# Kernel optimization log

Measured on AMD Instinct MI355X. Metric: run time of the kernel, lower is better.

The kernel has to match this reference:

```python
import jax, jax.numpy as jnp
import numpy as np

N_NODES = 1024; DEG = 24; K_NN = 12
C_S = 384; C_Z = 128; C_G = 16; N_RBF = 64
N_EDGES = N_NODES * DEG          # 24576
N_EE = N_EDGES * K_NN            # 294912 edge-edge pairs
LN_EPS = 1e-5
RBF_MIN, RBF_MAX = 0.0, 20.0


def _layernorm(x, w, b):
    m = x.mean(-1, keepdims=True)
    v = ((x - m) ** 2).mean(-1, keepdims=True)
    return (x - m) * jax.lax.rsqrt(v + LN_EPS) * w + b


def setup_inputs() -> dict:
    key = jax.random.key(0)
    ks = iter(jax.random.split(key, 40))

    def lin(i, o):
        w = jax.random.normal(next(ks), (i, o), jnp.float32) / np.sqrt(i)
        b = jax.random.normal(next(ks), (o,), jnp.float32) * 0.01
        return w, b

    node_features = jax.random.normal(next(ks), (N_NODES, C_S), jnp.float32)
    node_trans = jax.random.normal(next(ks), (N_NODES, 3), jnp.float32) * 10.0
    edge_features = jax.random.normal(next(ks), (N_EDGES, C_Z), jnp.float32)

    # edge_index sorted by destination (column 1), fixed in-degree DEG per node
    rng = np.random.default_rng(0)
    dst = np.repeat(np.arange(N_NODES), DEG)
    src = rng.integers(0, N_NODES, size=N_EDGES)
    edge_index = jnp.asarray(np.stack([src, dst]), jnp.int32)

    # edge-edge kNN graph: each edge paired with K_NN other edges sharing the
    # same destination node (mirrors knn_graph(..., batch=sorted_edge_index[1]))
    t = np.arange(N_EDGES)
    base = (t // DEG) * DEG
    off = t % DEG
    nbr = base[:, None] + (off[:, None] + 1 + np.arange(K_NN)[None, :]) % DEG  # [E,K]
    edge_edge_index = jnp.asarray(
        np.stack([nbr.reshape(-1), np.repeat(t, K_NN)]), jnp.int32)  # [2, N_EE]

    ln_w = jnp.ones((C_Z,), jnp.float32); ln_b = jnp.zeros((C_Z,), jnp.float32)
    wl_w, wl_b = lin(C_S, C_G)
    wr_w, wr_b = lin(C_S, C_G)
    ep_w, ep_b = lin(C_Z, C_Z)
    eg_w, eg_b = lin(C_Z, C_Z)
    dg_w, dg_b = lin(C_G * C_G, C_Z)
    dp_w, dp_b = lin(N_RBF, C_Z)
    lno_w = jnp.ones((C_Z,), jnp.float32); lno_b = jnp.zeros((C_Z,), jnp.float32)
    lo_w, lo_b = lin(C_Z, C_Z)
    og_w, og_b = lin(C_Z, C_Z)

    return dict(node_features=node_features, node_trans=node_trans,
                edge_features=edge_features,
                ln_w=ln_w, ln_b=ln_b, wl_w=wl_w, wl_b=wl_b, wr_w=wr_w, wr_b=wr_b,
                ep_w=ep_w, ep_b=ep_b, eg_w=eg_w, eg_b=eg_b,
                dg_w=dg_w, dg_b=dg_b, dp_w=dp_w, dp_b=dp_b,
                lno_w=lno_w, lno_b=lno_b, lo_w=lo_w, lo_b=lo_b,
                og_w=og_w, og_b=og_b,
                edge_index=edge_index, edge_edge_index=edge_edge_index)


def reference(node_features, node_trans, edge_features,
              ln_w, ln_b, wl_w, wl_b, wr_w, wr_b,
              ep_w, ep_b, eg_w, eg_b, dg_w, dg_b, dp_w, dp_b,
              lno_w, lno_b, lo_w, lo_b, og_w, og_b,
              edge_index, edge_edge_index):
    eps = 1e-8
    src = edge_index[0]
    eei0, eei1 = edge_edge_index[0], edge_edge_index[1]
    n1 = src[eei1]  # source node of target edge of each pair
    n2 = src[eei0]  # source node of source edge of each pair

    ef = _layernorm(edge_features, ln_w, ln_b)            # [E, c_z]
    nl = node_features @ wl_w + wl_b                      # [N, c_g]
    nr = node_features @ wr_w + wr_b                      # [N, c_g]

    # per-pair outer product, flattened: [N_EE, c_g*c_g]
    e3 = (nl[n1][:, :, None] * nr[n2][:, None, :]).reshape(-1, C_G * C_G)
    gate3 = e3 @ dg_w + dg_b                              # [N_EE, c_z]

    d = jnp.linalg.norm(node_trans[n1] - node_trans[n2] + eps, axis=-1)
    mu = jnp.linspace(RBF_MIN, RBF_MAX, N_RBF)
    sigma = (RBF_MAX - RBF_MIN) / N_RBF
    rbf = jnp.exp(-(((d[:, None] - mu) / sigma) ** 2))    # [N_EE, num_rbf]
    e3f = jax.nn.sigmoid(gate3) * (rbf @ dp_w + dp_b)

    e2 = jax.nn.sigmoid(ef @ eg_w + eg_b) * (ef @ ep_w + ep_b)  # [E, c_z]
    upd = e2[eei0] * e3f                                  # [N_EE, c_z]
    upd = jax.ops.segment_sum(upd, eei0, num_segments=N_EDGES)  # [E, c_z]

    upd = _layernorm(upd, lno_w, lno_b) @ lo_w + lo_b
    upd = upd * jax.nn.sigmoid(ef @ og_w + og_b)
    return upd
```

## Files before the change

kernel.cpp:

```cpp
#include <hip/hip_runtime.h>
#include <math.h>

#define N_NODES 1024
#define DEG     24
#define K_NN    12
#define C_S     384
#define C_Z     128
#define C_G     16
#define N_RBF   64
#define N_EDGES (N_NODES*DEG)

typedef short short8 __attribute__((ext_vector_type(8)));
typedef float f32x4  __attribute__((ext_vector_type(4)));

__device__ __forceinline__ float sigf(float x) {
  return __builtin_amdgcn_rcpf(1.f + __expf(-x));
}

__device__ __forceinline__ short f2b(float x) {
  union { float f; unsigned u; } v; v.f = x;
  unsigned r = v.u + 0x7FFFu + ((v.u >> 16) & 1u);
  return (short)(r >> 16);
}
__device__ __forceinline__ float b2f(short s) {
  union { unsigned u; float f; } v; v.u = ((unsigned)(unsigned short)s) << 16;
  return v.f;
}

__global__ __launch_bounds__(256) void k_prep(
    const float* __restrict__ nf, const float* __restrict__ wl_w, const float* __restrict__ wl_b,
    const float* __restrict__ wr_w, const float* __restrict__ wr_b,
    const float* __restrict__ dg_w,
    float* __restrict__ nl, short* __restrict__ At)
{
  __shared__ float rows[4][C_S];
  __shared__ float nrv[4][C_G];
  int b = blockIdx.x, t = threadIdx.x;
  for (int v = t; v < 4*C_S; v += 256) rows[v/C_S][v%C_S] = nf[(size_t)b*4*C_S + v];
  __syncthreads();
  {
    int nd = t >> 6, lt = t & 63;
    int c = lt >> 1, jseg = lt & 1, cc = c & 15;
    const float* w = (c < 16) ? wl_w : wr_w;
    float acc = 0.f;
    #pragma unroll 8
    for (int j = jseg*192; j < jseg*192 + 192; ++j) acc += rows[nd][j] * w[j*C_G + cc];
    acc += __shfl_xor(acc, 1);
    if (jseg == 0) {
      float v = acc + ((c < 16) ? wl_b[cc] : wr_b[cc]);
      if (c < 16) nl[(b*4 + nd)*C_G + cc] = v;
      else nrv[nd][cc] = v;
    }
  }
  __syncthreads();
  {
    int c2 = t & 127, ih = t >> 7;
    float a4[4][8];
    #pragma unroll
    for (int nd = 0; nd < 4; ++nd)
      #pragma unroll
      for (int q = 0; q < 8; ++q) a4[nd][q] = 0.f;
    for (int j = 0; j < C_G; ++j) {
      float w8[8];
      #pragma unroll
      for (int q = 0; q < 8; ++q) w8[q] = dg_w[(size_t)((ih*8 + q)*C_G + j)*C_Z + c2];
      #pragma unroll
      for (int nd = 0; nd < 4; ++nd) {
        float nv = nrv[nd][j];
        #pragma unroll
        for (int q = 0; q < 8; ++q) a4[nd][q] += nv * w8[q];
      }
    }
    #pragma unroll
    for (int nd = 0; nd < 4; ++nd) {
      short8 o8;
      #pragma unroll
      for (int q = 0; q < 8; ++q) o8[q] = f2b(a4[nd][q]);
      *(short8*)&At[(size_t)(b*4 + nd)*2048 + c2*16 + ih*8] = o8;
    }
  }
}

__global__ __launch_bounds__(256) void k_wts(
    const float* __restrict__ eg, const float* __restrict__ ep,
    const float* __restrict__ og, const float* __restrict__ lo,
    const float* __restrict__ dp_w,
    short* __restrict__ wT, short* __restrict__ dpT)
{
  int b = blockIdx.x, t = threadIdx.x;
  if (b == 64) {
    int c2 = t & 127, rh = t >> 7;
    for (int r = rh*36; r < rh*36 + 36; ++r)
      dpT[c2*72 + r] = (r < 64) ? f2b(dp_w[r*128 + c2]) : (short)0;
    return;
  }
  __shared__ float tb[32][33];
  int w = b >> 4; int tile = b & 15;
  int bi = tile >> 2, bj = tile & 3;
  const float* src = (w == 0) ? eg : (w == 1) ? ep : (w == 2) ? og : lo;
  short* dst = wT + w * 16384;
  int c = t & 31, r0 = t >> 5;
  #pragma unroll
  for (int p = 0; p < 4; ++p) { int r = r0 + p*8; tb[r][c] = src[(bi*32 + r)*128 + bj*32 + c]; }
  __syncthreads();
  #pragma unroll
  for (int p = 0; p < 4; ++p) { int r = r0 + p*8; dst[(bj*32 + r)*128 + bi*32 + c] = f2b(tb[c][r]); }
}

__global__ __launch_bounds__(384) void k_gates(
    const float* __restrict__ efin, const float* __restrict__ ln_w, const float* __restrict__ ln_b,
    const short* __restrict__ wT,
    const float* __restrict__ eg_b, const float* __restrict__ ep_b, const float* __restrict__ og_b,
    float* __restrict__ e2, short* __restrict__ ogs)
{
  __shared__ short xn[6*16*136];
  int t = threadIdx.x;
  int wv = t >> 6, lane = t & 63;
  int col = lane & 15, grp = lane >> 4;
  int ebase = blockIdx.x * 96 + wv * 16;
  int row = col, c0 = grp * 32;
  float x[32];
  {
    size_t ein = (size_t)(ebase + row) * C_Z + c0;
    #pragma unroll
    for (int q = 0; q < 8; ++q) {
      float4 v = *(const float4*)(efin + ein + q*4);
      x[q*4+0]=v.x; x[q*4+1]=v.y; x[q*4+2]=v.z; x[q*4+3]=v.w;
    }
  }
  float s = 0.f;
  #pragma unroll
  for (int q = 0; q < 32; ++q) s += x[q];
  s += __shfl_xor(s, 16); s += __shfl_xor(s, 32);
  float mean = s * (1.f/128.f);
  float vs = 0.f;
  #pragma unroll
  for (int q = 0; q < 32; ++q) { float d = x[q]-mean; vs += d*d; }
  vs += __shfl_xor(vs, 16); vs += __shfl_xor(vs, 32);
  float rstd = rsqrtf(vs*(1.f/128.f) + 1e-5f);
  short* xw = &xn[wv*2176 + row*136 + c0];
  #pragma unroll
  for (int h = 0; h < 4; ++h) {
    short8 o;
    #pragma unroll
    for (int j = 0; j < 8; ++j) {
      int idx = h*8 + j;
      o[j] = f2b((x[idx]-mean)*rstd*ln_w[c0+idx] + ln_b[c0+idx]);
    }
    *(short8*)(xw + h*8) = o;
  }
  __syncthreads();
  short8 a[4];
  const short* xr = &xn[wv*2176 + col*136];
  #pragma unroll
  for (int ks = 0; ks < 4; ++ks) a[ks] = *(const short8*)(xr + ks*32 + grp*8);
  #pragma unroll
  for (int h = 0; h < 8; ++h) {
    int ch = col + 16*h;
    f32x4 acc = (f32x4){0.f,0.f,0.f,0.f}, acc2 = (f32x4){0.f,0.f,0.f,0.f};
    #pragma unroll
    for (int ks = 0; ks < 4; ++ks)
      acc = __builtin_amdgcn_mfma_f32_16x16x32_bf16(
          a[ks], *(const short8*)(wT + (size_t)ch*128 + ks*32 + grp*8), acc, 0, 0, 0);
    #pragma unroll
    for (int ks = 0; ks < 4; ++ks)
      acc2 = __builtin_amdgcn_mfma_f32_16x16x32_bf16(
          a[ks], *(const short8*)(wT + 16384 + (size_t)ch*128 + ks*32 + grp*8), acc2, 0, 0, 0);
    float egb = eg_b[ch], epb = ep_b[ch];
    #pragma unroll
    for (int r = 0; r < 4; ++r) {
      size_t e = (size_t)(ebase + grp*4 + r);
      e2[e*C_Z + ch] = sigf(acc[r] + egb) * (acc2[r] + epb);
    }
  }
  #pragma unroll
  for (int h = 0; h < 8; ++h) {
    int ch = col + 16*h;
    f32x4 acc = (f32x4){0.f,0.f,0.f,0.f};
    #pragma unroll
    for (int ks = 0; ks < 4; ++ks)
      acc = __builtin_amdgcn_mfma_f32_16x16x32_bf16(
          a[ks], *(const short8*)(wT + 32768 + (size_t)ch*128 + ks*32 + grp*8), acc, 0, 0, 0);
    float ogb = og_b[ch];
    #pragma unroll
    for (int r = 0; r < 4; ++r) {
      size_t e = (size_t)(ebase + grp*4 + r);
      ogs[e*C_Z + ch] = f2b(sigf(acc[r] + ogb));
    }
  }
}

__global__ __launch_bounds__(256) void k_pairs2(
    const int* __restrict__ eidx, const float* __restrict__ pos,
    const float* __restrict__ nl, const short* __restrict__ At, const short* __restrict__ dpTg,
    const float* __restrict__ dg_b, const float* __restrict__ dp_b,
    const float* __restrict__ e2, const float* __restrict__ lno_w, const float* __restrict__ lno_b,
    short* __restrict__ Un)
{
  __shared__ float p4[DEG][4];
  __shared__ int   s24[DEG];
  __shared__ short nlb[DEG*C_G];
  int t = threadIdx.x;
  int g = blockIdx.x / 6, sub = blockIdx.x - g*6;
  if (t < DEG) {
    int s = eidx[g*DEG + t];
    s24[t] = s;
    p4[t][0] = pos[s*3+0]; p4[t][1] = pos[s*3+1]; p4[t][2] = pos[s*3+2]; p4[t][3] = 0.f;
  }
  __syncthreads();
  for (int v = t; v < DEG*C_G; v += 256)
    nlb[v] = f2b(nl[s24[v>>4]*C_G + (v & 15)]);
  __syncthreads();

  int wv = t >> 6, lane = t & 63, col = lane & 15, grp = lane >> 4;
  int o = sub*4 + wv;

  float dgb[8], dpb[8];
  #pragma unroll
  for (int q = 0; q < 8; ++q) { int c = col+16*q; dgb[q] = dg_b[c]; dpb[q] = dp_b[c]; }
  const float RS = 3.2f, MUS = 20.f/63.f;

  int n2 = s24[o];
  int o2 = o - 1 - col; if (o2 < 0) o2 += DEG;
  bool vk = (col < K_NN);
  float d;
  {
    float dx = p4[o2][0]-p4[o][0]+1e-8f;
    float dy = p4[o2][1]-p4[o][1]+1e-8f;
    float dz = p4[o2][2]-p4[o][2]+1e-8f;
    d = vk ? sqrtf(dx*dx+dy*dy+dz*dz) : 1.0e6f;
  }
  short8 zz = {0,0,0,0,0,0,0,0};
  short8 a_nl = zz;
  if (vk && grp < 2) a_nl = *(const short8*)&nlb[o2*C_G + grp*8];
  short8 a_r0, a_r1;
  #pragma unroll
  for (int j = 0; j < 8; ++j) {
    float z0 = (d - (float)(grp*8 + j)*MUS)*RS;
    float z1 = (d - (float)(32 + grp*8 + j)*MUS)*RS;
    a_r0[j] = f2b(__expf(-z0*z0));
    a_r1[j] = f2b(__expf(-z1*z1));
  }
  const short8* Ab = (const short8*)(At + (size_t)n2*2048);
  float v1 = 0.f, v2 = 0.f;
  #pragma unroll
  for (int cb = 0; cb < 8; ++cb) {
    f32x4 accg = (f32x4){0.f,0.f,0.f,0.f};
    f32x4 accd = (f32x4){0.f,0.f,0.f,0.f};
    short8 b = (grp < 2) ? Ab[(col+16*cb)*2 + grp] : zz;
    accg = __builtin_amdgcn_mfma_f32_16x16x32_bf16(a_nl, b, accg, 0, 0, 0);
    const short* dbase = dpTg + (col+16*cb)*72 + grp*8;
    accd = __builtin_amdgcn_mfma_f32_16x16x32_bf16(a_r0, *(const short8*)dbase,      accd, 0, 0, 0);
    accd = __builtin_amdgcn_mfma_f32_16x16x32_bf16(a_r1, *(const short8*)(dbase+32), accd, 0, 0, 0);
    float sacc = 0.f;
    #pragma unroll
    for (int r = 0; r < 4; ++r)
      sacc += sigf(accg[r] + dgb[cb]) * (accd[r] + dpb[cb]);
    sacc = (grp == 3) ? 0.f : sacc;
    sacc += __shfl_xor(sacc, 16); sacc += __shfl_xor(sacc, 32);
    v1 = (cb == grp)     ? sacc : v1;
    v2 = (cb == grp + 4) ? sacc : v2;
  }
  size_t e = (size_t)(g*DEG + o);
  v1 *= e2[e*C_Z + lane];
  v2 *= e2[e*C_Z + 64 + lane];
  float s = v1 + v2;
  s += __shfl_xor(s,1); s += __shfl_xor(s,2); s += __shfl_xor(s,4);
  s += __shfl_xor(s,8); s += __shfl_xor(s,16); s += __shfl_xor(s,32);
  float mean = s * (1.f/128.f);
  float d1 = v1 - mean, d2 = v2 - mean;
  float vsum = d1*d1 + d2*d2;
  vsum += __shfl_xor(vsum,1); vsum += __shfl_xor(vsum,2); vsum += __shfl_xor(vsum,4);
  vsum += __shfl_xor(vsum,8); vsum += __shfl_xor(vsum,16); vsum += __shfl_xor(vsum,32);
  float rstd = rsqrtf(vsum*(1.f/128.f) + 1e-5f);
  Un[e*C_Z + lane]      = f2b(d1*rstd*lno_w[lane]      + lno_b[lane]);
  Un[e*C_Z + 64 + lane] = f2b(d2*rstd*lno_w[64 + lane] + lno_b[64 + lane]);
}

__global__ __launch_bounds__(256) void k_out2(
    const short* __restrict__ Un, const short* __restrict__ wTlo, const float* __restrict__ lo_b,
    const short* __restrict__ ogs, float* __restrict__ out)
{
  int t = threadIdx.x, wv = t >> 6, lane = t & 63, col = lane & 15, grp = lane >> 4;
  int ebase = blockIdx.x * 64 + wv * 16;
  short8 ua[4];
  #pragma unroll
  for (int ks = 0; ks < 4; ++ks)
    ua[ks] = *(const short8*)(Un + (size_t)(ebase + col)*C_Z + ks*32 + grp*8);
  #pragma unroll
  for (int h = 0; h < 8; ++h) {
    int ch = col + 16*h;
    f32x4 oacc = (f32x4){0.f,0.f,0.f,0.f};
    #pragma unroll
    for (int ks = 0; ks < 4; ++ks)
      oacc = __builtin_amdgcn_mfma_f32_16x16x32_bf16(
          ua[ks], *(const short8*)(wTlo + (size_t)ch*128 + ks*32 + grp*8), oacc, 0, 0, 0);
    float lob = lo_b[ch];
    #pragma unroll
    for (int r = 0; r < 4; ++r) {
      size_t e = (size_t)(ebase + grp*4 + r);
      out[e*C_Z + ch] = (oacc[r] + lob) * b2f(ogs[e*C_Z + ch]);
    }
  }
}

extern "C" void kernel_launch(void* const* d_in, const int* in_sizes, int n_in,
                              void* d_out, int out_size, void* d_ws, size_t ws_size,
                              hipStream_t stream)
{
  const float* nf    = (const float*)d_in[0];
  const float* pos   = (const float*)d_in[1];
  const float* efin  = (const float*)d_in[2];
  const float* ln_w  = (const float*)d_in[3];
  const float* ln_b  = (const float*)d_in[4];
  const float* wl_w  = (const float*)d_in[5];
  const float* wl_b  = (const float*)d_in[6];
  const float* wr_w  = (const float*)d_in[7];
  const float* wr_b  = (const float*)d_in[8];
  const float* ep_w  = (const float*)d_in[9];
  const float* ep_b  = (const float*)d_in[10];
  const float* eg_w  = (const float*)d_in[11];
  const float* eg_b  = (const float*)d_in[12];
  const float* dg_w  = (const float*)d_in[13];
  const float* dg_b  = (const float*)d_in[14];
  const float* dp_w  = (const float*)d_in[15];
  const float* dp_b  = (const float*)d_in[16];
  const float* lno_w = (const float*)d_in[17];
  const float* lno_b = (const float*)d_in[18];
  const float* lo_w  = (const float*)d_in[19];
  const float* lo_b  = (const float*)d_in[20];
  const float* og_w  = (const float*)d_in[21];
  const float* og_b  = (const float*)d_in[22];
  const int*   eidx  = (const int*)d_in[23];

  float* ws   = (float*)d_ws;
  float* nlw  = ws;
  short* Atw  = (short*)(ws + 32768);
  short* dpTw = (short*)(ws + 32768 + 1048576);
  short* wTw  = (short*)(ws + 32768 + 1048576 + 8192);
  float* e2w  = ws + 1122304;
  short* ogw  = (short*)(ws + 4268032);
  short* Unw  = (short*)(ws + 5840896);
  float* outp = (float*)d_out;

  k_prep  <<<256, 256, 0, stream>>>(nf, wl_w, wl_b, wr_w, wr_b, dg_w, nlw, Atw);
  k_wts   <<<65, 256, 0, stream>>>(eg_w, ep_w, og_w, lo_w, dp_w, wTw, dpTw);
  k_gates <<<256, 384, 0, stream>>>(efin, ln_w, ln_b, wTw, eg_b, ep_b, og_b, e2w, ogw);
  k_pairs2<<<6144, 256, 0, stream>>>(eidx, pos, nlw, Atw, dpTw, dg_b, dp_b,
                                     e2w, lno_w, lno_b, Unw);
  k_out2  <<<384, 256, 0, stream>>>(Unw, wTw + 49152, lo_b, ogw, outp);
}
```

Measured before the change: 113.5 us.

## Fuse edge gates, pair aggregation and output projection into one kernel

Merges the gating kernel, pair kernel and output kernel into a single per-edge kernel. Each block of 4 edges does its input layernorm, the eg/ep/og projections, the pair aggregation and the output projection, keeping intermediates in shared memory. This removes the global round trips for e2, og and Un plus two launches. The cost is that the MFMA tiles now use only 4 of 16 rows, wasting matrix throughput and reloading the weight matrices per block. The nl buffer is also stored as bf16.

```diff
diff --git a/kernel.cpp b/kernel.cpp
--- a/kernel.cpp
+++ b/kernel.cpp
@@ -31,7 +31,7 @@
     const float* __restrict__ nf, const float* __restrict__ wl_w, const float* __restrict__ wl_b,
     const float* __restrict__ wr_w, const float* __restrict__ wr_b,
     const float* __restrict__ dg_w,
-    float* __restrict__ nl, short* __restrict__ At)
+    short* __restrict__ nlB, short* __restrict__ At)
 {
   __shared__ float rows[4][C_S];
   __shared__ float nrv[4][C_G];
@@ -48,7 +48,7 @@
     acc += __shfl_xor(acc, 1);
     if (jseg == 0) {
       float v = acc + ((c < 16) ? wl_b[cc] : wr_b[cc]);
-      if (c < 16) nl[(b*4 + nd)*C_G + cc] = v;
+      if (c < 16) nlB[(b*4 + nd)*C_G + cc] = f2b(v);
       else nrv[nd][cc] = v;
     }
   }
@@ -107,101 +107,29 @@
   for (int p = 0; p < 4; ++p) { int r = r0 + p*8; dst[(bj*32 + r)*128 + bi*32 + c] = f2b(tb[c][r]); }
 }
 
-__global__ __launch_bounds__(384) void k_gates(
+__global__ __launch_bounds__(256) void k_mega(
     const float* __restrict__ efin, const float* __restrict__ ln_w, const float* __restrict__ ln_b,
     const short* __restrict__ wT,
     const float* __restrict__ eg_b, const float* __restrict__ ep_b, const float* __restrict__ og_b,
-    float* __restrict__ e2, short* __restrict__ ogs)
+    const int* __restrict__ eidx, const float* __restrict__ pos,
+    const short* __restrict__ nlB, const short* __restrict__ At, const short* __restrict__ dpTg,
+    const float* __restrict__ dg_b, const float* __restrict__ dp_b,
+    const float* __restrict__ lno_w, const float* __restrict__ lno_b, const float* __restrict__ lo_b,
+    float* __restrict__ out)
 {
-  __shared__ short xn[6*16*136];
-  int t = threadIdx.x;
-  int wv = t >> 6, lane = t & 63;
-  int col = lane & 15, grp = lane >> 4;
-  int ebase = blockIdx.x * 96 + wv * 16;
-  int row = col, c0 = grp * 32;
-  float x[32];
-  {
-    size_t ein = (size_t)(ebase + row) * C_Z + c0;
-    #pragma unroll
-    for (int q = 0; q < 8; ++q) {
-      float4 v = *(const float4*)(efin + ein + q*4);
-      x[q*4+0]=v.x; x[q*4+1]=v.y; x[q*4+2]=v.z; x[q*4+3]=v.w;
-    }
-  }
-  float s = 0.f;
-  #pragma unroll
-  for (int q = 0; q < 32; ++q) s += x[q];
-  s += __shfl_xor(s, 16); s += __shfl_xor(s, 32);
-  float mean = s * (1.f/128.f);
-  float vs = 0.f;
-  #pragma unroll
-  for (int q = 0; q < 32; ++q) { float d = x[q]-mean; vs += d*d; }
-  vs += __shfl_xor(vs, 16); vs += __shfl_xor(vs, 32);
-  float rstd = rsqrtf(vs*(1.f/128.f) + 1e-5f);
-  short* xw = &xn[wv*2176 + row*136 + c0];
-  #pragma unroll
-  for (int h = 0; h < 4; ++h) {
-    short8 o;
-    #pragma unroll
-    for (int j = 0; j < 8; ++j) {
-      int idx = h*8 + j;
-      o[j] = f2b((x[idx]-mean)*rstd*ln_w[c0+idx] + ln_b[c0+idx]);
-    }
-    *(short8*)(xw + h*8) = o;
-  }
-  __syncthreads();
-  short8 a[4];
-  const short* xr = &xn[wv*2176 + col*136];
-  #pragma unroll
-  for (int ks = 0; ks < 4; ++ks) a[ks] = *(const short8*)(xr + ks*32 + grp*8);
-  #pragma unroll
-  for (int h = 0; h < 8; ++h) {
-    int ch = col + 16*h;
-    f32x4 acc = (f32x4){0.f,0.f,0.f,0.f}, acc2 = (f32x4){0.f,0.f,0.f,0.f};
-    #pragma unroll
-    for (int ks = 0; ks < 4; ++ks)
-      acc = __builtin_amdgcn_mfma_f32_16x16x32_bf16(
-          a[ks], *(const short8*)(wT + (size_t)ch*128 + ks*32 + grp*8), acc, 0, 0, 0);
-    #pragma unroll
-    for (int ks = 0; ks < 4; ++ks)
-      acc2 = __builtin_amdgcn_mfma_f32_16x16x32_bf16(
-          a[ks], *(const short8*)(wT + 16384 + (size_t)ch*128 + ks*32 + grp*8), acc2, 0, 0, 0);
-    float egb = eg_b[ch], epb = ep_b[ch];
-    #pragma unroll
-    for (int r = 0; r < 4; ++r) {
-      size_t e = (size_t)(ebase + grp*4 + r);
-      e2[e*C_Z + ch] = sigf(acc[r] + egb) * (acc2[r] + epb);
-    }
-  }
-  #pragma unroll
-  for (int h = 0; h < 8; ++h) {
-    int ch = col + 16*h;
-    f32x4 acc = (f32x4){0.f,0.f,0.f,0.f};
-    #pragma unroll
-    for (int ks = 0; ks < 4; ++ks)
-      acc = __builtin_amdgcn_mfma_f32_16x16x32_bf16(
-          a[ks], *(const short8*)(wT + 32768 + (size_t)ch*128 + ks*32 + grp*8), acc, 0, 0, 0);
-    float ogb = og_b[ch];
-    #pragma unroll
-    for (int r = 0; r < 4; ++r) {
-      size_t e = (size_t)(ebase + grp*4 + r);
-      ogs[e*C_Z + ch] = f2b(sigf(acc[r] + ogb));
-    }
-  }
-}
-
-__global__ __launch_bounds__(256) void k_pairs2(
-    const int* __restrict__ eidx, const float* __restrict__ pos,
-    const float* __restrict__ nl, const short* __restrict__ At, const short* __restrict__ dpTg,
-    const float* __restrict__ dg_b, const float* __restrict__ dp_b,
-    const float* __restrict__ e2, const float* __restrict__ lno_w, const float* __restrict__ lno_b,
-    short* __restrict__ Un)
-{
+  __shared__ short xn[4][136];
+  __shared__ float e2s[4][128];
+  __shared__ short ogss[4][128];
   __shared__ float p4[DEG][4];
   __shared__ int   s24[DEG];
   __shared__ short nlb[DEG*C_G];
+
   int t = threadIdx.x;
   int g = blockIdx.x / 6, sub = blockIdx.x - g*6;
+  int wv = t >> 6, lane = t & 63, col = lane & 15, grp = lane >> 4;
+  int o = sub*4 + wv;
+  size_t e = (size_t)g*DEG + o;
+
   if (t < DEG) {
     int s = eidx[g*DEG + t];
     s24[t] = s;
@@ -209,97 +137,137 @@
   }
   __syncthreads();
   for (int v = t; v < DEG*C_G; v += 256)
-    nlb[v] = f2b(nl[s24[v>>4]*C_G + (v & 15)]);
-  __syncthreads();
-
-  int wv = t >> 6, lane = t & 63, col = lane & 15, grp = lane >> 4;
-  int o = sub*4 + wv;
-
-  float dgb[8], dpb[8];
-  #pragma unroll
-  for (int q = 0; q < 8; ++q) { int c = col+16*q; dgb[q] = dg_b[c]; dpb[q] = dp_b[c]; }
-  const float RS = 3.2f, MUS = 20.f/63.f;
-
-  int n2 = s24[o];
-  int o2 = o - 1 - col; if (o2 < 0) o2 += DEG;
-  bool vk = (col < K_NN);
-  float d;
-  {
-    float dx = p4[o2][0]-p4[o][0]+1e-8f;
-    float dy = p4[o2][1]-p4[o][1]+1e-8f;
-    float dz = p4[o2][2]-p4[o][2]+1e-8f;
-    d = vk ? sqrtf(dx*dx+dy*dy+dz*dz) : 1.0e6f;
-  }
+    nlb[v] = nlB[s24[v>>4]*C_G + (v & 15)];
+
+  {
+    float x1 = efin[e*C_Z + lane], x2 = efin[e*C_Z + 64 + lane];
+    float s = x1 + x2;
+    s += __shfl_xor(s,1); s += __shfl_xor(s,2); s += __shfl_xor(s,4);
+    s += __shfl_xor(s,8); s += __shfl_xor(s,16); s += __shfl_xor(s,32);
+    float mean = s * (1.f/128.f);
+    float d1 = x1 - mean, d2 = x2 - mean;
+    float vs = d1*d1 + d2*d2;
+    vs += __shfl_xor(vs,1); vs += __shfl_xor(vs,2); vs += __shfl_xor(vs,4);
+    vs += __shfl_xor(vs,8); vs += __shfl_xor(vs,16); vs += __shfl_xor(vs,32);
+    float rstd = rsqrtf(vs*(1.f/128.f) + 1e-5f);
+    xn[wv][lane]      = f2b(d1*rstd*ln_w[lane]      + ln_b[lane]);
+    xn[wv][64 + lane] = f2b(d2*rstd*ln_w[64 + lane] + ln_b[64 + lane]);
+  }
+  __syncthreads();
+
   short8 zz = {0,0,0,0,0,0,0,0};
-  short8 a_nl = zz;
-  if (vk && grp < 2) a_nl = *(const short8*)&nlb[o2*C_G + grp*8];
-  short8 a_r0, a_r1;
-  #pragma unroll
-  for (int j = 0; j < 8; ++j) {
-    float z0 = (d - (float)(grp*8 + j)*MUS)*RS;
-    float z1 = (d - (float)(32 + grp*8 + j)*MUS)*RS;
-    a_r0[j] = f2b(__expf(-z0*z0));
-    a_r1[j] = f2b(__expf(-z1*z1));
-  }
-  const short8* Ab = (const short8*)(At + (size_t)n2*2048);
-  float v1 = 0.f, v2 = 0.f;
-  #pragma unroll
-  for (int cb = 0; cb < 8; ++cb) {
-    f32x4 accg = (f32x4){0.f,0.f,0.f,0.f};
-    f32x4 accd = (f32x4){0.f,0.f,0.f,0.f};
-    short8 b = (grp < 2) ? Ab[(col+16*cb)*2 + grp] : zz;
-    accg = __builtin_amdgcn_mfma_f32_16x16x32_bf16(a_nl, b, accg, 0, 0, 0);
-    const short* dbase = dpTg + (col+16*cb)*72 + grp*8;
-    accd = __builtin_amdgcn_mfma_f32_16x16x32_bf16(a_r0, *(const short8*)dbase,      accd, 0, 0, 0);
-    accd = __builtin_amdgcn_mfma_f32_16x16x32_bf16(a_r1, *(const short8*)(dbase+32), accd, 0, 0, 0);
-    float sacc = 0.f;
-    #pragma unroll
-    for (int r = 0; r < 4; ++r)
-      sacc += sigf(accg[r] + dgb[cb]) * (accd[r] + dpb[cb]);
-    sacc = (grp == 3) ? 0.f : sacc;
-    sacc += __shfl_xor(sacc, 16); sacc += __shfl_xor(sacc, 32);
-    v1 = (cb == grp)     ? sacc : v1;
-    v2 = (cb == grp + 4) ? sacc : v2;
-  }
-  size_t e = (size_t)(g*DEG + o);
-  v1 *= e2[e*C_Z + lane];
-  v2 *= e2[e*C_Z + 64 + lane];
-  float s = v1 + v2;
-  s += __shfl_xor(s,1); s += __shfl_xor(s,2); s += __shfl_xor(s,4);
-  s += __shfl_xor(s,8); s += __shfl_xor(s,16); s += __shfl_xor(s,32);
-  float mean = s * (1.f/128.f);
-  float d1 = v1 - mean, d2 = v2 - mean;
-  float vsum = d1*d1 + d2*d2;
-  vsum += __shfl_xor(vsum,1); vsum += __shfl_xor(vsum,2); vsum += __shfl_xor(vsum,4);
-  vsum += __shfl_xor(vsum,8); vsum += __shfl_xor(vsum,16); vsum += __shfl_xor(vsum,32);
-  float rstd = rsqrtf(vsum*(1.f/128.f) + 1e-5f);
-  Un[e*C_Z + lane]      = f2b(d1*rstd*lno_w[lane]      + lno_b[lane]);
-  Un[e*C_Z + 64 + lane] = f2b(d2*rstd*lno_w[64 + lane] + lno_b[64 + lane]);
-}
-
-__global__ __launch_bounds__(256) void k_out2(
-    const short* __restrict__ Un, const short* __restrict__ wTlo, const float* __restrict__ lo_b,
-    const short* __restrict__ ogs, float* __restrict__ out)
-{
-  int t = threadIdx.x, wv = t >> 6, lane = t & 63, col = lane & 15, grp = lane >> 4;
-  int ebase = blockIdx.x * 64 + wv * 16;
-  short8 ua[4];
-  #pragma unroll
-  for (int ks = 0; ks < 4; ++ks)
-    ua[ks] = *(const short8*)(Un + (size_t)(ebase + col)*C_Z + ks*32 + grp*8);
-  #pragma unroll
-  for (int h = 0; h < 8; ++h) {
-    int ch = col + 16*h;
-    f32x4 oacc = (f32x4){0.f,0.f,0.f,0.f};
+
+  {
+    short8 a[4];
     #pragma unroll
     for (int ks = 0; ks < 4; ++ks)
-      oacc = __builtin_amdgcn_mfma_f32_16x16x32_bf16(
-          ua[ks], *(const short8*)(wTlo + (size_t)ch*128 + ks*32 + grp*8), oacc, 0, 0, 0);
-    float lob = lo_b[ch];
-    #pragma unroll
-    for (int r = 0; r < 4; ++r) {
-      size_t e = (size_t)(ebase + grp*4 + r);
-      out[e*C_Z + ch] = (oacc[r] + lob) * b2f(ogs[e*C_Z + ch]);
+      a[ks] = (col < 4) ? *(const short8*)&xn[col][ks*32 + grp*8] : zz;
+    #pragma unroll
+    for (int h = 0; h < 2; ++h) {
+      int ch = col + 16*(wv*2 + h);
+      f32x4 aE = (f32x4){0.f,0.f,0.f,0.f}, aP = aE, aO = aE;
+      #pragma unroll
+      for (int ks = 0; ks < 4; ++ks) {
+        aE = __builtin_amdgcn_mfma_f32_16x16x32_bf16(
+            a[ks], *(const short8*)(wT + (size_t)ch*128 + ks*32 + grp*8), aE, 0, 0, 0);
+        aP = __builtin_amdgcn_mfma_f32_16x16x32_bf16(
+            a[ks], *(const short8*)(wT + 16384 + (size_t)ch*128 + ks*32 + grp*8), aP, 0, 0, 0);
+        aO = __builtin_amdgcn_mfma_f32_16x16x32_bf16(
+            a[ks], *(const short8*)(wT + 32768 + (size_t)ch*128 + ks*32 + grp*8), aO, 0, 0, 0);
+      }
+      if (grp == 0) {
+        float egb = eg_b[ch], epb = ep_b[ch], ogb = og_b[ch];
+        #pragma unroll
+        for (int r = 0; r < 4; ++r) {
+          e2s[r][ch]  = sigf(aE[r] + egb) * (aP[r] + epb);
+          ogss[r][ch] = f2b(sigf(aO[r] + ogb));
+        }
+      }
+    }
+  }
+  __syncthreads();
+
+  {
+    float dgb[8], dpb[8];
+    #pragma unroll
+    for (int q = 0; q < 8; ++q) { int c = col+16*q; dgb[q] = dg_b[c]; dpb[q] = dp_b[c]; }
+    const float RS = 3.2f, MUS = 20.f/63.f;
+
+    int n2 = s24[o];
+    int o2 = o - 1 - col; if (o2 < 0) o2 += DEG;
+    bool vk = (col < K_NN);
+    float d;
+    {
+      float dx = p4[o2][0]-p4[o][0]+1e-8f;
+      float dy = p4[o2][1]-p4[o][1]+1e-8f;
+      float dz = p4[o2][2]-p4[o][2]+1e-8f;
+      d = vk ? sqrtf(dx*dx+dy*dy+dz*dz) : 1.0e6f;
+    }
+    short8 a_nl = zz;
+    if (vk && grp < 2) a_nl = *(const short8*)&nlb[o2*C_G + grp*8];
+    short8 a_r0, a_r1;
+    #pragma unroll
+    for (int j = 0; j < 8; ++j) {
+      float z0 = (d - (float)(grp*8 + j)*MUS)*RS;
+      float z1 = (d - (float)(32 + grp*8 + j)*MUS)*RS;
+      a_r0[j] = f2b(__expf(-z0*z0));
+      a_r1[j] = f2b(__expf(-z1*z1));
+    }
+    const short8* Ab = (const short8*)(At + (size_t)n2*2048);
+    float v1 = 0.f, v2 = 0.f;
+    #pragma unroll
+    for (int cb = 0; cb < 8; ++cb) {
+      f32x4 accg = (f32x4){0.f,0.f,0.f,0.f};
+      f32x4 accd = (f32x4){0.f,0.f,0.f,0.f};
+      short8 b = (grp < 2) ? Ab[(col+16*cb)*2 + grp] : zz;
+      accg = __builtin_amdgcn_mfma_f32_16x16x32_bf16(a_nl, b, accg, 0, 0, 0);
+      const short* dbase = dpTg + (col+16*cb)*72 + grp*8;
+      accd = __builtin_amdgcn_mfma_f32_16x16x32_bf16(a_r0, *(const short8*)dbase,      accd, 0, 0, 0);
+      accd = __builtin_amdgcn_mfma_f32_16x16x32_bf16(a_r1, *(const short8*)(dbase+32), accd, 0, 0, 0);
+      float sacc = 0.f;
+      #pragma unroll
+      for (int r = 0; r < 4; ++r)
+        sacc += sigf(accg[r] + dgb[cb]) * (accd[r] + dpb[cb]);
+      sacc = (grp == 3) ? 0.f : sacc;
+      sacc += __shfl_xor(sacc, 16); sacc += __shfl_xor(sacc, 32);
+      v1 = (cb == grp)     ? sacc : v1;
+      v2 = (cb == grp + 4) ? sacc : v2;
+    }
+    v1 *= e2s[wv][lane];
+    v2 *= e2s[wv][64 + lane];
+    float s = v1 + v2;
+    s += __shfl_xor(s,1); s += __shfl_xor(s,2); s += __shfl_xor(s,4);
+    s += __shfl_xor(s,8); s += __shfl_xor(s,16); s += __shfl_xor(s,32);
+    float mean = s * (1.f/128.f);
+    float d1 = v1 - mean, d2 = v2 - mean;
+    float vsum = d1*d1 + d2*d2;
+    vsum += __shfl_xor(vsum,1); vsum += __shfl_xor(vsum,2); vsum += __shfl_xor(vsum,4);
+    vsum += __shfl_xor(vsum,8); vsum += __shfl_xor(vsum,16); vsum += __shfl_xor(vsum,32);
+    float rstd = rsqrtf(vsum*(1.f/128.f) + 1e-5f);
+    xn[wv][lane]      = f2b(d1*rstd*lno_w[lane]      + lno_b[lane]);
+    xn[wv][64 + lane] = f2b(d2*rstd*lno_w[64 + lane] + lno_b[64 + lane]);
+  }
+  __syncthreads();
+
+  {
+    short8 ua[4];
+    #pragma unroll
+    for (int ks = 0; ks < 4; ++ks)
+      ua[ks] = (col < 4) ? *(const short8*)&xn[col][ks*32 + grp*8] : zz;
+    #pragma unroll
+    for (int h = 0; h < 2; ++h) {
+      int ch = col + 16*(wv*2 + h);
+      f32x4 oacc = (f32x4){0.f,0.f,0.f,0.f};
+      #pragma unroll
+      for (int ks = 0; ks < 4; ++ks)
+        oacc = __builtin_amdgcn_mfma_f32_16x16x32_bf16(
+            ua[ks], *(const short8*)(wT + 49152 + (size_t)ch*128 + ks*32 + grp*8), oacc, 0, 0, 0);
+      if (grp == 0) {
+        float lob = lo_b[ch];
+        #pragma unroll
+        for (int r = 0; r < 4; ++r)
+          out[(size_t)(g*DEG + sub*4 + r)*C_Z + ch] = (oacc[r] + lob) * b2f(ogss[r][ch]);
+      }
     }
   }
 }
@@ -334,19 +302,15 @@
   const int*   eidx  = (const int*)d_in[23];
 
   float* ws   = (float*)d_ws;
-  float* nlw  = ws;
+  short* nlBw = (short*)ws;
   short* Atw  = (short*)(ws + 32768);
   short* dpTw = (short*)(ws + 32768 + 1048576);
   short* wTw  = (short*)(ws + 32768 + 1048576 + 8192);
-  float* e2w  = ws + 1122304;
-  short* ogw  = (short*)(ws + 4268032);
-  short* Unw  = (short*)(ws + 5840896);
   float* outp = (float*)d_out;
 
-  k_prep  <<<256, 256, 0, stream>>>(nf, wl_w, wl_b, wr_w, wr_b, dg_w, nlw, Atw);
-  k_wts   <<<65, 256, 0, stream>>>(eg_w, ep_w, og_w, lo_w, dp_w, wTw, dpTw);
-  k_gates <<<256, 384, 0, stream>>>(efin, ln_w, ln_b, wTw, eg_b, ep_b, og_b, e2w, ogw);
-  k_pairs2<<<6144, 256, 0, stream>>>(eidx, pos, nlw, Atw, dpTw, dg_b, dp_b,
-                                     e2w, lno_w, lno_b, Unw);
-  k_out2  <<<384, 256, 0, stream>>>(Unw, wTw + 49152, lo_b, ogw, outp);
-}
+  k_prep <<<256, 256, 0, stream>>>(nf, wl_w, wl_b, wr_w, wr_b, dg_w, nlBw, Atw);
+  k_wts  <<<65, 256, 0, stream>>>(eg_w, ep_w, og_w, lo_w, dp_w, wTw, dpTw);
+  k_mega <<<6144, 256, 0, stream>>>(efin, ln_w, ln_b, wTw, eg_b, ep_b, og_b,
+                                    eidx, pos, nlBw, Atw, dpTw, dg_b, dp_b,
+                                    lno_w, lno_b, lo_b, outp);
+}
```

New measurement: 155.3 us. 1.37x slower.
